# Optimization experiments

Hardware: AMD Instinct MI355X
Metric: run time of the kernel (lower is better)

The kernel has to match this reference:

```python
import jax, jax.numpy as jnp
import numpy as np

FEATURES = 8
POINTS = 3
CLASSES = 128
BATCH = 1024
TEMPERATURE = 0.1


def setup_inputs() -> dict:
    key = jax.random.key(0)
    k1, k2, k3 = jax.random.split(key, 3)
    x = jax.random.normal(k1, (BATCH, FEATURES), dtype=jnp.float32)
    beta = jax.random.uniform(k2, (FEATURES, POINTS), dtype=jnp.float32)
    classifier = jax.random.uniform(
        k3, ((POINTS + 1) ** FEATURES, CLASSES), dtype=jnp.float32)
    return {"x": x, "beta": beta, "classifier": classifier}


def reference(x, beta, classifier):
    # b: sort beta ascending per-feature, negate, cumsum, prepend a zero bin edge
    T = 1.0 / TEMPERATURE
    bneg = jnp.cumsum(-jnp.sort(beta, axis=1), axis=1)            # [F, P]
    b = jnp.concatenate(
        [jnp.zeros((beta.shape[0], 1), beta.dtype), bneg], axis=1)  # [F, P+1]
    w = jnp.arange(1, POINTS + 2, dtype=x.dtype)                  # [P+1]
    # soft one-hot binning per feature: [B, F, P+1]
    logits = (x[:, :, None] * w[None, None, :] + b[None, :, :]) * T
    hot = jax.nn.softmax(logits, axis=-1)
    # iterative outer product over features -> joint leaf histogram [B, (P+1)^F]
    B = x.shape[0]
    leaves = hot[:, 0, :]
    for f in range(1, FEATURES):  # small fixed loop over features
        leaves = (leaves[:, :, None] * hot[:, f, None, :]).reshape(B, -1)
    return leaves @ classifier  # [B, classes]
```

## Files before the change

### kernel.cpp

```cpp
#include <hip/hip_runtime.h>
#include <stdint.h>

typedef unsigned short u16;
typedef __attribute__((ext_vector_type(4))) float f32x4;
typedef __attribute__((ext_vector_type(2))) float f32x2;
typedef __attribute__((ext_vector_type(8))) short s16x8;

#define T_INV 10.0f

__device__ __forceinline__ u16 f2bf(float f) {
  uint32_t u = __float_as_uint(f);
  uint32_t r = (u + 0x7FFFu + ((u >> 16) & 1u)) >> 16;
  return (u16)r;
}

__device__ __forceinline__ void gload_lds16(const void* g, void* l) {
  __builtin_amdgcn_global_load_lds(
      (const __attribute__((address_space(1))) uint32_t*)(g),
      (__attribute__((address_space(3))) uint32_t*)(l),
      16, 0, 0);
}

__global__ __launch_bounds__(256) void k_tables(
    const float* __restrict__ x, const float* __restrict__ beta,
    u16* __restrict__ plo, float* __restrict__ phi)
{
  const int t = threadIdx.x;
  const int b = blockIdx.x * 64 + (t >> 2);
  const int q = t & 3;

  float hot[8][4];
#pragma unroll
  for (int f = 0; f < 8; ++f) {
    float b0 = beta[f*3+0], b1 = beta[f*3+1], b2 = beta[f*3+2];
    float s0 = fminf(b0, fminf(b1, b2));
    float s2 = fmaxf(b0, fmaxf(b1, b2));
    float s1 = b0 + b1 + b2 - s0 - s2;
    float bv1 = -s0, bv2 = -(s0 + s1), bv3 = -(s0 + s1 + s2);
    float xf = x[b*8 + f];
    float l0 = (xf * 1.0f       ) * T_INV;
    float l1 = (xf * 2.0f + bv1) * T_INV;
    float l2 = (xf * 3.0f + bv2) * T_INV;
    float l3 = (xf * 4.0f + bv3) * T_INV;
    float mm = fmaxf(fmaxf(l0, l1), fmaxf(l2, l3));
    float e0 = __expf(l0 - mm), e1 = __expf(l1 - mm);
    float e2 = __expf(l2 - mm), e3 = __expf(l3 - mm);
    float inv = 1.0f / (e0 + e1 + e2 + e3);
    hot[f][0] = e0*inv; hot[f][1] = e1*inv; hot[f][2] = e2*inv; hot[f][3] = e3*inv;
  }

  {
    float h23[16];
#pragma unroll
    for (int i2 = 0; i2 < 4; ++i2)
#pragma unroll
      for (int i3 = 0; i3 < 4; ++i3) h23[i2*4+i3] = hot[2][i2] * hot[3][i3];
    float h0q = hot[0][q];
    float* dst = phi + (size_t)b*256 + q*64;
#pragma unroll
    for (int i1 = 0; i1 < 4; ++i1) {
      float c01 = h0q * hot[1][i1];
#pragma unroll
      for (int j = 0; j < 16; j += 4) {
        f32x4 v;
        v.x = c01 * h23[j+0]; v.y = c01 * h23[j+1];
        v.z = c01 * h23[j+2]; v.w = c01 * h23[j+3];
        *(f32x4*)(dst + i1*16 + j) = v;
      }
    }
  }
  {
    float h67[16];
#pragma unroll
    for (int i6 = 0; i6 < 4; ++i6)
#pragma unroll
      for (int i7 = 0; i7 < 4; ++i7) h67[i6*4+i7] = hot[6][i6] * hot[7][i7];
    float h4q = hot[4][q];
    u16* dst = plo + (size_t)b*256 + q*64;
#pragma unroll
    for (int i5 = 0; i5 < 4; ++i5) {
      float c45 = h4q * hot[5][i5];
#pragma unroll
      for (int j = 0; j < 16; j += 8) {
        s16x8 v;
#pragma unroll
        for (int e = 0; e < 8; ++e) v[e] = (short)f2bf(c45 * h67[j+e]);
        *(s16x8*)(dst + i5*16 + j) = v;
      }
    }
  }
}

__global__ __launch_bounds__(256) void k_transpose(
    const float* __restrict__ cls, u16* __restrict__ ct)
{
  __shared__ float tile[64 * 132];
  const int t = threadIdx.x;
  const int k0 = blockIdx.x * 64;
#pragma unroll
  for (int it = 0; it < 8; ++it) {
    int e = it * 1024 + t * 4;
    int r = e >> 7;
    int c = e & 127;
    f32x4 v = *(const f32x4*)(cls + (size_t)(k0 + r) * 128 + c);
    *(f32x4*)(tile + r * 132 + c) = v;
  }
  __syncthreads();
  const int c  = t >> 1;
  const int kh = t & 1;
  u16 vals[32];
#pragma unroll
  for (int j = 0; j < 32; ++j)
    vals[j] = f2bf(tile[(kh*32 + j) * 132 + c]);
  u16* dst = ct + (size_t)c * 65536 + k0 + kh * 32;
#pragma unroll
  for (int qq = 0; qq < 4; ++qq) {
    s16x8 v;
#pragma unroll
    for (int e2 = 0; e2 < 8; ++e2) v[e2] = (short)vals[qq*8 + e2];
    *(s16x8*)(dst + qq*8) = v;
  }
}

__global__ __launch_bounds__(512, 4) void k_main(
    const u16* __restrict__ plo, const float* __restrict__ phi,
    const u16* __restrict__ ct, u16* __restrict__ pws)
{
  __shared__ __align__(16) u16 Ab[2][4096];
  __shared__ __align__(16) u16 Bb[2][4096];
  __shared__ __align__(16) float Ph[512];

  const int wg  = blockIdx.x;
  const int xcd = wg & 7;
  const int idx = wg >> 3;
  const int hig = xcd * 8 + (idx >> 3);
  const int m   = idx & 7;

  const int t    = threadIdx.x;
  const int l    = t & 63;
  const int w    = t >> 6;
  const int lrow = l & 15;
  const int kg   = l >> 4;
  const int rbase = (w & 1) * 64;
  const int cbase = (w >> 1) * 32;

  if (t < 128) {
    f32x4 v = *(const f32x4*)(phi + (size_t)(m*128 + t) * 256 + hig * 4);
    *(f32x4*)(Ph + t * 4) = v;
  }

  const u16* ploM = plo + (size_t)m * 128 * 256;
  const int srow = t >> 2;
  const int ssl  = t & 3;
  const int sg   = (ssl - ((srow >> 1) & 3)) & 3;

  f32x4 acc[4][2], hacc[4][2];
#pragma unroll
  for (int i = 0; i < 4; ++i)
#pragma unroll
    for (int j = 0; j < 2; ++j) { acc[i][j] = (f32x4)0.0f; hacc[i][j] = (f32x4)0.0f; }

  auto stage = [&](int h, int ks, int buf) {
    gload_lds16(ploM + (size_t)srow * 256 + ks * 32 + sg * 8, &Ab[buf][t * 8]);
    int k0 = (hig * 4 + h) * 256 + ks * 32;
    gload_lds16(ct + (size_t)srow * 65536 + k0 + sg * 8, &Bb[buf][t * 8]);
  };

  stage(0, 0, 0);
  __syncthreads();

#pragma unroll 1
  for (int h = 0; h < 4; ++h) {
#pragma unroll
    for (int ks = 0; ks < 8; ++ks) {
      const int buf = ks & 1;
      if (h < 3 || ks < 7) {
        int nks = (ks + 1) & 7;
        int nh  = h + (ks == 7);
        stage(nh, nks, buf ^ 1);
      }
      s16x8 afr[4], bfr[2];
#pragma unroll
      for (int mt = 0; mt < 4; ++mt) {
        int row = rbase + mt * 16 + lrow;
        int s = (kg + ((row >> 1) & 3)) & 3;
        afr[mt] = *(const s16x8*)&Ab[buf][row * 32 + s * 8];
      }
#pragma unroll
      for (int nt = 0; nt < 2; ++nt) {
        int c = cbase + nt * 16 + lrow;
        int s = (kg + ((c >> 1) & 3)) & 3;
        bfr[nt] = *(const s16x8*)&Bb[buf][c * 32 + s * 8];
      }
#pragma unroll
      for (int mt = 0; mt < 4; ++mt)
#pragma unroll
        for (int nt = 0; nt < 2; ++nt)
          hacc[mt][nt] = __builtin_amdgcn_mfma_f32_16x16x32_bf16(
              afr[mt], bfr[nt], hacc[mt][nt], 0, 0, 0);
      __syncthreads();
    }
#pragma unroll
    for (int mt = 0; mt < 4; ++mt) {
#pragma unroll
      for (int r = 0; r < 4; ++r) {
        float p = Ph[(rbase + mt * 16 + kg * 4 + r) * 4 + h];
#pragma unroll
        for (int nt = 0; nt < 2; ++nt)
          acc[mt][nt][r] += p * hacc[mt][nt][r];
      }
#pragma unroll
      for (int nt = 0; nt < 2; ++nt) hacc[mt][nt] = (f32x4)0.0f;
    }
  }

  u16* dst = pws + ((size_t)hig * 1024 + (size_t)m * 128) * 128;
#pragma unroll
  for (int mt = 0; mt < 4; ++mt)
#pragma unroll
    for (int r = 0; r < 4; ++r) {
      int row = rbase + mt * 16 + kg * 4 + r;
#pragma unroll
      for (int nt = 0; nt < 2; ++nt) {
        int col = cbase + nt * 16 + lrow;
        dst[row * 128 + col] = f2bf(acc[mt][nt][r]);
      }
    }
}

__global__ __launch_bounds__(256) void k_reduce(
    const u16* __restrict__ p, float* __restrict__ out)
{
  const int g = blockIdx.x * 256 + threadIdx.x;
  const u16* src = p + (size_t)g * 2;
  float a0 = 0.0f, a1 = 0.0f;
#pragma unroll 8
  for (int hig = 0; hig < 64; ++hig) {
    uint32_t v = *(const uint32_t*)(src + (size_t)hig * 131072);
    a0 += __uint_as_float((v & 0xFFFFu) << 16);
    a1 += __uint_as_float(v & 0xFFFF0000u);
  }
  f32x2 o; o.x = a0; o.y = a1;
  *(f32x2*)(out + (size_t)g * 2) = o;
}

extern "C" void kernel_launch(void* const* d_in, const int* in_sizes, int n_in,
                              void* d_out, int out_size, void* d_ws, size_t ws_size,
                              hipStream_t stream)
{
  const float* x    = (const float*)d_in[0];
  const float* beta = (const float*)d_in[1];
  const float* cls  = (const float*)d_in[2];
  float* out = (float*)d_out;

  char* ws = (char*)d_ws;
  u16*   ct  = (u16*)ws;
  u16*   plo = (u16*)(ws + (16u << 20));
  float* phi = (float*)(ws + (16u << 20) + 524288);
  u16*   pws = (u16*)(ws + (16u << 20) + 524288 + 1048576);

  k_tables<<<16, 256, 0, stream>>>(x, beta, plo, phi);
  k_transpose<<<1024, 256, 0, stream>>>(cls, ct);
  k_main<<<512, 512, 0, stream>>>(plo, phi, ct, pws);
  k_reduce<<<256, 256, 0, stream>>>(pws, out);
}
```

Measured before the change: 53.59 us.

## Keep full A tile resident in LDS and read transposed phi directly

k_main now loads all eight A k-slices from plo into LDS once up front instead of reloading the same A slice for each of the four h iterations. Only the classifier B tile is still double-buffered. The phi table is written transposed by k_tables so k_main can read four per-row scale factors as one vector straight from global memory instead of staging them in LDS. LDS use per block grows from about 34 KB to about 80 KB, which may reduce the number of resident blocks per CU. The phi writes in k_tables become scattered scalar stores.

Measured after the change: 49.42 us. -7.8%, faster.

```diff
diff --git a/kernel.cpp b/kernel.cpp
--- a/kernel.cpp
+++ b/kernel.cpp
@@ -23,7 +23,7 @@
 
 __global__ __launch_bounds__(256) void k_tables(
     const float* __restrict__ x, const float* __restrict__ beta,
-    u16* __restrict__ plo, float* __restrict__ phi)
+    u16* __restrict__ plo, float* __restrict__ phiT)
 {
   const int t = threadIdx.x;
   const int b = blockIdx.x * 64 + (t >> 2);
@@ -56,17 +56,12 @@
 #pragma unroll
       for (int i3 = 0; i3 < 4; ++i3) h23[i2*4+i3] = hot[2][i2] * hot[3][i3];
     float h0q = hot[0][q];
-    float* dst = phi + (size_t)b*256 + q*64;
 #pragma unroll
     for (int i1 = 0; i1 < 4; ++i1) {
       float c01 = h0q * hot[1][i1];
 #pragma unroll
-      for (int j = 0; j < 16; j += 4) {
-        f32x4 v;
-        v.x = c01 * h23[j+0]; v.y = c01 * h23[j+1];
-        v.z = c01 * h23[j+2]; v.w = c01 * h23[j+3];
-        *(f32x4*)(dst + i1*16 + j) = v;
-      }
+      for (int j = 0; j < 16; ++j)
+        phiT[(size_t)(q*64 + i1*16 + j) * 1024 + b] = c01 * h23[j];
     }
   }
   {
@@ -123,12 +118,11 @@
 }
 
 __global__ __launch_bounds__(512, 4) void k_main(
-    const u16* __restrict__ plo, const float* __restrict__ phi,
+    const u16* __restrict__ plo, const float* __restrict__ phiT,
     const u16* __restrict__ ct, u16* __restrict__ pws)
 {
-  __shared__ __align__(16) u16 Ab[2][4096];
+  __shared__ __align__(16) u16 As[8][4096];
   __shared__ __align__(16) u16 Bb[2][4096];
-  __shared__ __align__(16) float Ph[512];
 
   const int wg  = blockIdx.x;
   const int xcd = wg & 7;
@@ -144,30 +138,28 @@
   const int rbase = (w & 1) * 64;
   const int cbase = (w >> 1) * 32;
 
-  if (t < 128) {
-    f32x4 v = *(const f32x4*)(phi + (size_t)(m*128 + t) * 256 + hig * 4);
-    *(f32x4*)(Ph + t * 4) = v;
-  }
-
   const u16* ploM = plo + (size_t)m * 128 * 256;
   const int srow = t >> 2;
   const int ssl  = t & 3;
   const int sg   = (ssl - ((srow >> 1) & 3)) & 3;
 
-  f32x4 acc[4][2], hacc[4][2];
-#pragma unroll
-  for (int i = 0; i < 4; ++i)
-#pragma unroll
-    for (int j = 0; j < 2; ++j) { acc[i][j] = (f32x4)0.0f; hacc[i][j] = (f32x4)0.0f; }
-
-  auto stage = [&](int h, int ks, int buf) {
-    gload_lds16(ploM + (size_t)srow * 256 + ks * 32 + sg * 8, &Ab[buf][t * 8]);
+#pragma unroll
+  for (int ks = 0; ks < 8; ++ks)
+    gload_lds16(ploM + (size_t)srow * 256 + ks * 32 + sg * 8, &As[ks][t * 8]);
+
+  auto stageB = [&](int h, int ks, int buf) {
     int k0 = (hig * 4 + h) * 256 + ks * 32;
     gload_lds16(ct + (size_t)srow * 65536 + k0 + sg * 8, &Bb[buf][t * 8]);
   };
 
-  stage(0, 0, 0);
+  stageB(0, 0, 0);
   __syncthreads();
+
+  f32x4 acc[4][2], hacc[4][2];
+#pragma unroll
+  for (int i = 0; i < 4; ++i)
+#pragma unroll
+    for (int j = 0; j < 2; ++j) { acc[i][j] = (f32x4)0.0f; hacc[i][j] = (f32x4)0.0f; }
 
 #pragma unroll 1
   for (int h = 0; h < 4; ++h) {
@@ -177,14 +169,14 @@
       if (h < 3 || ks < 7) {
         int nks = (ks + 1) & 7;
         int nh  = h + (ks == 7);
-        stage(nh, nks, buf ^ 1);
+        stageB(nh, nks, buf ^ 1);
       }
       s16x8 afr[4], bfr[2];
 #pragma unroll
       for (int mt = 0; mt < 4; ++mt) {
         int row = rbase + mt * 16 + lrow;
         int s = (kg + ((row >> 1) & 3)) & 3;
-        afr[mt] = *(const s16x8*)&Ab[buf][row * 32 + s * 8];
+        afr[mt] = *(const s16x8*)&As[ks][row * 32 + s * 8];
       }
 #pragma unroll
       for (int nt = 0; nt < 2; ++nt) {
@@ -200,14 +192,15 @@
               afr[mt], bfr[nt], hacc[mt][nt], 0, 0, 0);
       __syncthreads();
     }
+    const float* ph = phiT + (size_t)(hig * 4 + h) * 1024 + m * 128;
 #pragma unroll
     for (int mt = 0; mt < 4; ++mt) {
+      f32x4 p4 = *(const f32x4*)(ph + rbase + mt * 16 + kg * 4);
 #pragma unroll
       for (int r = 0; r < 4; ++r) {
-        float p = Ph[(rbase + mt * 16 + kg * 4 + r) * 4 + h];
 #pragma unroll
         for (int nt = 0; nt < 2; ++nt)
-          acc[mt][nt][r] += p * hacc[mt][nt][r];
+          acc[mt][nt][r] += p4[r] * hacc[mt][nt][r];
       }
 #pragma unroll
       for (int nt = 0; nt < 2; ++nt) hacc[mt][nt] = (f32x4)0.0f;
@@ -254,13 +247,13 @@
   float* out = (float*)d_out;
 
   char* ws = (char*)d_ws;
-  u16*   ct  = (u16*)ws;
-  u16*   plo = (u16*)(ws + (16u << 20));
-  float* phi = (float*)(ws + (16u << 20) + 524288);
-  u16*   pws = (u16*)(ws + (16u << 20) + 524288 + 1048576);
-
-  k_tables<<<16, 256, 0, stream>>>(x, beta, plo, phi);
+  u16*   ct   = (u16*)ws;
+  u16*   plo  = (u16*)(ws + (16u << 20));
+  float* phiT = (float*)(ws + (16u << 20) + 524288);
+  u16*   pws  = (u16*)(ws + (16u << 20) + 524288 + 1048576);
+
+  k_tables<<<16, 256, 0, stream>>>(x, beta, plo, phiT);
   k_transpose<<<1024, 256, 0, stream>>>(cls, ct);
-  k_main<<<512, 512, 0, stream>>>(plo, phi, ct, pws);
+  k_main<<<512, 512, 0, stream>>>(plo, phiT, ct, pws);
   k_reduce<<<256, 256, 0, stream>>>(pws, out);
 }
```
